# Optimization experiments

Measured on AMD Instinct MI355X. Metric: run time of the kernel, lower is better.

Reference implementation:

```python
import jax, jax.numpy as jnp
import numpy as np

B, S, D = 4, 4096, 1024
H = 16
HD = D // H
L = 4
MLP_MULT = 4
MAX_CHUNKS = 1024
ROPE_BASE = 10000.0


def _rms(x):
    eps = jnp.asarray(jnp.finfo(x.dtype).eps, x.dtype)
    return x * jax.lax.rsqrt(jnp.mean(x * x, axis=-1, keepdims=True) + eps)


def _rope_tables(seq_len, dim):
    inv = 1.0 / ROPE_BASE ** (np.arange(0, dim, 2, dtype=np.float32) / dim)
    t = np.arange(seq_len, dtype=np.float32)
    freqs = np.outer(t, inv)  # [T, dim/2]
    return jnp.asarray(np.cos(freqs)), jnp.asarray(np.sin(freqs))


def _apply_rope(x, cos, sin):
    # x: [B,H,T,hd]; cos/sin: [T, hd/2]
    half = x.shape[-1] // 2
    x1, x2 = x[..., :half], x[..., half:]
    c = cos[None, None, :, :]
    s = sin[None, None, :, :]
    return jnp.concatenate([x1 * c + x2 * s, -x1 * s + x2 * c], axis=-1)


def chunk_reduce(x, boundary_hard, max_chunks):
    # x: [B,S,D]; boundary_hard: [B,S] in {0,1}, boundary_hard[:,0]==1
    ids = jnp.cumsum(boundary_hard.astype(jnp.int32), axis=1) - 1  # [B,S]
    seg = lambda xb, ib: jax.ops.segment_sum(xb, ib, num_segments=max_chunks)
    sums = jax.vmap(seg)(x, ids)                                   # [B,C,D]
    counts = jax.vmap(seg)(jnp.ones(x.shape[:2], x.dtype)[..., None].swapaxes(0, 0), ids) if False else jax.vmap(seg)(jnp.ones((x.shape[0], x.shape[1], 1), x.dtype), ids)
    latents = sums / jnp.maximum(counts, 1.0)
    num_chunks = ids[:, -1] + 1
    valid = jnp.arange(max_chunks)[None, :] < num_chunks[:, None]
    return latents, ids, valid


def _attn(x, wq, wk, wv, wo, qg, cos, sin):
    b, t, _ = x.shape
    q = (x @ wq.T).reshape(b, t, H, HD).transpose(0, 2, 1, 3)
    k = (x @ wk.T).reshape(b, t, H, HD).transpose(0, 2, 1, 3)
    v = (x @ wv.T).reshape(b, t, H, HD).transpose(0, 2, 1, 3)
    q = _apply_rope(_rms(q), cos, sin)
    k = _apply_rope(_rms(k), cos, sin)
    q = q * qg[None, :, None, None]
    scores = jnp.einsum('bhqd,bhkd->bhqk', q, k) / np.sqrt(HD).astype(np.float32)
    causal = jnp.tril(jnp.ones((t, t), bool))
    scores = jnp.where(causal[None, None], scores, jnp.asarray(-jnp.inf, scores.dtype))
    p = jax.nn.softmax(scores, axis=-1)
    y = jnp.einsum('bhqk,bhkd->bhqd', p, v).transpose(0, 2, 1, 3).reshape(b, t, D)
    return y @ wo.T


def _mlp(x, fc, proj):
    h = jax.nn.relu(x @ fc.T)
    return (h * h) @ proj.T


def reference(x, boundary_hard, Wq, Wk, Wv, Wo, q_gain, fc_w, proj_w,
              attn_scale, mlp_scale, resid_mix, max_chunks):
    latents, _, valid = chunk_reduce(x, boundary_hard, max_chunks)
    cos, sin = _rope_tables(max_chunks, HD)
    x0 = latents
    h = latents
    for l in range(L):
        mix = resid_mix[l]
        h = mix[0][None, None, :] * h + mix[1][None, None, :] * x0
        a = _attn(_rms(h), Wq[l], Wk[l], Wv[l], Wo[l], q_gain[l], cos, sin)
        h = h + attn_scale[l][None, None, :] * a
        h = h + mlp_scale[l][None, None, :] * _mlp(_rms(h), fc_w[l], proj_w[l])
    return h * valid[..., None].astype(h.dtype)


def setup_inputs() -> dict:
    key = jax.random.key(0)
    ks = jax.random.split(key, 12)
    rng = np.random.default_rng(0)
    boundary = np.zeros((B, S), np.int32)
    for b in range(B):
        kcnt = int(rng.integers(MAX_CHUNKS // 2, MAX_CHUNKS - 1))
        pos = rng.choice(S, size=kcnt, replace=False)
        boundary[b, pos] = 1
    boundary[:, 0] = 1
    sd = 0.02
    return {
        'x': jax.random.normal(ks[0], (B, S, D), jnp.float32),
        'boundary_hard': jnp.asarray(boundary),
        'Wq': jax.random.normal(ks[1], (L, D, D), jnp.float32) * sd,
        'Wk': jax.random.normal(ks[2], (L, D, D), jnp.float32) * sd,
        'Wv': jax.random.normal(ks[3], (L, D, D), jnp.float32) * sd,
        'Wo': jax.random.normal(ks[4], (L, D, D), jnp.float32) * sd,
        'q_gain': jnp.ones((L, H), jnp.float32),
        'fc_w': jax.random.normal(ks[5], (L, MLP_MULT * D, D), jnp.float32) * sd,
        'proj_w': jax.random.normal(ks[6], (L, D, MLP_MULT * D), jnp.float32) * sd,
        'attn_scale': jnp.ones((L, D), jnp.float32),
        'mlp_scale': jnp.ones((L, D), jnp.float32),
        'resid_mix': jnp.stack([jnp.ones((L, D)), jnp.zeros((L, D))], axis=1).astype(jnp.float32),
        'max_chunks': MAX_CHUNKS,
    }
```

## Files before the change

kernel.cpp:

```cpp
#include <hip/hip_runtime.h>
#include <math.h>

#define BB   4
#define SS   4096
#define DD   1024
#define HH   16
#define HDIM 64
#define CC   1024
#define DFF  4096
#define LL   4

static constexpr float F32_EPS = 1.1920928955078125e-07f;

typedef __attribute__((ext_vector_type(8))) __bf16 bf16x8;
typedef __attribute__((ext_vector_type(4))) float  f32x4;

__device__ __forceinline__ uint f2bf(float f) {
    uint u = __float_as_uint(f);
    return (u + 0x7fffu + ((u >> 16) & 1u)) >> 16;
}
__device__ __forceinline__ float bf2f(uint u) {
    return __uint_as_float(u << 16);
}

__device__ __forceinline__ void gl_lds16(const ushort* g, ushort* l) {
    __builtin_amdgcn_global_load_lds(
        (const __attribute__((address_space(1))) unsigned int*)g,
        (__attribute__((address_space(3))) unsigned int*)l, 16, 0, 0);
}

__global__ __launch_bounds__(256) void castlayer_kernel(const float* __restrict__ Wq,
                                                        const float* __restrict__ Wk,
                                                        const float* __restrict__ Wv,
                                                        const float* __restrict__ Wo,
                                                        const float* __restrict__ fc,
                                                        const float* __restrict__ proj,
                                                        ushort* __restrict__ out) {
    int i = blockIdx.x * blockDim.x + threadIdx.x;
    const int U = DD * DD / 8;
    const float* src;
    if (i < 3 * U) {
        src = (i < U ? Wq : (i < 2 * U ? Wk : Wv)) + (size_t)(i < U ? i : (i < 2*U ? i-U : i-2*U)) * 8;
    } else if (i < 4 * U) {
        src = Wo + (size_t)(i - 3 * U) * 8;
    } else if (i < 8 * U) {
        src = fc + (size_t)(i - 4 * U) * 8;
    } else {
        src = proj + (size_t)(i - 8 * U) * 8;
    }
    const float4* p = (const float4*)src;
    float4 a = p[0], b = p[1];
    uint4 o;
    o.x = f2bf(a.x) | (f2bf(a.y) << 16);
    o.y = f2bf(a.z) | (f2bf(a.w) << 16);
    o.z = f2bf(b.x) | (f2bf(b.y) << 16);
    o.w = f2bf(b.z) | (f2bf(b.w) << 16);
    *(uint4*)(out + (size_t)i * 8) = o;
}

__global__ void rope_init_kernel(float* __restrict__ cosT, float* __restrict__ sinT) {
    int idx = blockIdx.x * blockDim.x + threadIdx.x;
    int pos = idx >> 5;
    int i   = idx & 31;
    float inv = powf(10000.0f, -(float)i / 32.0f);
    float f = (float)pos * inv;
    cosT[idx] = cosf(f);
    sinT[idx] = sinf(f);
}

__global__ __launch_bounds__(1024) void scan_kernel(const int* __restrict__ boundary,
                                                    int* __restrict__ starts,
                                                    int* __restrict__ nch) {
    __shared__ int tmp[1024];
    int b = blockIdx.x, t = threadIdx.x;
    int base = b * SS + t * 4;
    int v0 = boundary[base + 0], v1 = boundary[base + 1];
    int v2 = boundary[base + 2], v3 = boundary[base + 3];
    int p0 = v0, p1 = p0 + v1, p2 = p1 + v2, p3 = p2 + v3;
    tmp[t] = p3;
    __syncthreads();
    for (int off = 1; off < 1024; off <<= 1) {
        int add = (t >= off) ? tmp[t - off] : 0;
        __syncthreads();
        tmp[t] += add;
        __syncthreads();
    }
    int excl = tmp[t] - p3;
    if (v0) starts[b * (CC + 1) + (excl + p0 - 1)] = t * 4 + 0;
    if (v1) starts[b * (CC + 1) + (excl + p1 - 1)] = t * 4 + 1;
    if (v2) starts[b * (CC + 1) + (excl + p2 - 1)] = t * 4 + 2;
    if (v3) starts[b * (CC + 1) + (excl + p3 - 1)] = t * 4 + 3;
    int total = tmp[1023];
    if (t == 0) nch[b] = total;
    for (int c = t; c <= CC; c += 1024)
        if (c >= total) starts[b * (CC + 1) + c] = SS;
}

__global__ __launch_bounds__(256) void latents_kernel(const float* __restrict__ x,
                                                      const int* __restrict__ starts,
                                                      float* __restrict__ h,
                                                      float* __restrict__ x0) {
    int c = blockIdx.x, b = blockIdx.y, t = threadIdx.x;
    int s0 = starts[b * (CC + 1) + c];
    int s1 = starts[b * (CC + 1) + c + 1];
    float a0 = 0.f, a1 = 0.f, a2 = 0.f, a3 = 0.f;
    for (int r = s0; r < s1; ++r) {
        const float4 xv = *(const float4*)&x[((size_t)(b * SS + r)) * DD + t * 4];
        a0 += xv.x; a1 += xv.y; a2 += xv.z; a3 += xv.w;
    }
    float inv = (s1 > s0) ? 1.0f / (float)(s1 - s0) : 0.0f;
    float4 o = make_float4(a0 * inv, a1 * inv, a2 * inv, a3 * inv);
    size_t off = ((size_t)(b * CC + c)) * DD + t * 4;
    *(float4*)&h[off]  = o;
    *(float4*)&x0[off] = o;
}

__global__ __launch_bounds__(256) void rmsmix_kernel(const float* __restrict__ hin,
                                                     const float* __restrict__ x0,
                                                     const float* __restrict__ mix,
                                                     float* __restrict__ hout,
                                                     ushort* __restrict__ xnout) {
    int row = blockIdx.x, t = threadIdx.x;
    size_t off = (size_t)row * DD + t * 4;
    float4 hv = *(const float4*)&hin[off];
    float4 m0 = *(const float4*)&mix[t * 4];
    float4 m1 = *(const float4*)&mix[DD + t * 4];
    float4 xv = *(const float4*)&x0[off];
    hv.x = m0.x * hv.x + m1.x * xv.x;
    hv.y = m0.y * hv.y + m1.y * xv.y;
    hv.z = m0.z * hv.z + m1.z * xv.z;
    hv.w = m0.w * hv.w + m1.w * xv.w;
    float ss = hv.x * hv.x + hv.y * hv.y + hv.z * hv.z + hv.w * hv.w;
    for (int o = 32; o; o >>= 1) ss += __shfl_xor(ss, o);
    __shared__ float wsum[4];
    int lane = t & 63, wid = t >> 6;
    if (lane == 0) wsum[wid] = ss;
    __syncthreads();
    float tot = wsum[0] + wsum[1] + wsum[2] + wsum[3];
    float r = rsqrtf(tot * (1.0f / DD) + F32_EPS);
    *(float4*)&hout[off] = hv;
    uint2 pk;
    pk.x = f2bf(hv.x * r) | (f2bf(hv.y * r) << 16);
    pk.y = f2bf(hv.z * r) | (f2bf(hv.w * r) << 16);
    *(uint2*)&xnout[off] = pk;
}

template <int HASMIX>
__global__ __launch_bounds__(256) void residrms_kernel(float* __restrict__ h,
                                                       const ushort* __restrict__ a0,
                                                       const ushort* __restrict__ a1,
                                                       const float* __restrict__ scale,
                                                       const float* __restrict__ x0,
                                                       const float* __restrict__ mix,
                                                       ushort* __restrict__ xnout) {
    int row = blockIdx.x, t = threadIdx.x;
    size_t off = (size_t)row * DD + t * 4;
    float4 hv = *(const float4*)&h[off];
    uint2 pa = *(const uint2*)&a0[off];
    uint2 pb = *(const uint2*)&a1[off];
    float4 sv = *(const float4*)&scale[t * 4];
    hv.x += sv.x * (bf2f(pa.x & 0xffff) + bf2f(pb.x & 0xffff));
    hv.y += sv.y * (bf2f(pa.x >> 16)    + bf2f(pb.x >> 16));
    hv.z += sv.z * (bf2f(pa.y & 0xffff) + bf2f(pb.y & 0xffff));
    hv.w += sv.w * (bf2f(pa.y >> 16)    + bf2f(pb.y >> 16));
    if (HASMIX) {
        float4 m0 = *(const float4*)&mix[t * 4];
        float4 m1 = *(const float4*)&mix[DD + t * 4];
        float4 xv = *(const float4*)&x0[off];
        hv.x = m0.x * hv.x + m1.x * xv.x;
        hv.y = m0.y * hv.y + m1.y * xv.y;
        hv.z = m0.z * hv.z + m1.z * xv.z;
        hv.w = m0.w * hv.w + m1.w * xv.w;
    }
    float ss = hv.x * hv.x + hv.y * hv.y + hv.z * hv.z + hv.w * hv.w;
    for (int o = 32; o; o >>= 1) ss += __shfl_xor(ss, o);
    __shared__ float wsum[4];
    int lane = t & 63, wid = t >> 6;
    if (lane == 0) wsum[wid] = ss;
    __syncthreads();
    float tot = wsum[0] + wsum[1] + wsum[2] + wsum[3];
    float r = rsqrtf(tot * (1.0f / DD) + F32_EPS);
    *(float4*)&h[off] = hv;
    uint2 pk;
    pk.x = f2bf(hv.x * r) | (f2bf(hv.y * r) << 16);
    pk.y = f2bf(hv.z * r) | (f2bf(hv.w * r) << 16);
    *(uint2*)&xnout[off] = pk;
}

template <int EPI>
__global__ __launch_bounds__(256) void gemm_bf16(const ushort* __restrict__ A,
                                                 const ushort* __restrict__ W,
                                                 ushort* __restrict__ C0,
                                                 ushort* __restrict__ C1,
                                                 ushort* __restrict__ C2,
                                                 int M, int N, int K, int lda, int ldw,
                                                 size_t partStride) {
    __shared__ __align__(16) ushort Als[2][128 * 64];
    __shared__ __align__(16) ushort Wls[2][128 * 64];
    const int tid  = threadIdx.x;
    const int wid  = tid >> 6, lane = tid & 63;
    const int wr   = wid >> 1, wc   = wid & 1;
    const int l15  = lane & 15, lhi = lane >> 4;

    const int gx = gridDim.x, gy = gridDim.y;
    int i = (blockIdx.z * gy + blockIdx.y) * gx + blockIdx.x;
    int G = gx * gy * (int)gridDim.z;
    int v = (i & 7) * (G >> 3) + (i >> 3);
    int mt = v % gy;
    int rest = v / gy;
    int nt = rest % gx;
    int zt = rest / gx;
    const int mbase = mt * 128, nbase = nt * 128;

    A  += (size_t)zt * K;
    W  += (size_t)zt * K;
    C0 += (size_t)zt * partStride;

    const int srow8  = lane >> 3;
    const int gchunk = ((lane & 7) ^ srow8) * 8;
    const ushort* Ag = A + (size_t)(mbase + wid * 32 + srow8) * lda + gchunk;
    const ushort* Wg = W + (size_t)(nbase + wid * 32 + srow8) * ldw + gchunk;
    const int ldsoff = (wid * 32) * 64;

    f32x4 acc[4][4] = {};
    const int swz  = (l15 & 7) << 3;
    const int aoff = (wr * 64 + l15) * 64;
    const int woff = (wc * 64 + l15) * 64;

    auto STAGE = [&](ushort* Alb, ushort* Wlb, int kk) {
#pragma unroll
        for (int s = 0; s < 4; ++s) {
            gl_lds16(Ag + kk + (size_t)s * 8 * lda, Alb + ldsoff + s * 8 * 64);
            gl_lds16(Wg + kk + (size_t)s * 8 * ldw, Wlb + ldsoff + s * 8 * 64);
        }
    };
    auto COMPUTE = [&](const ushort* Ab, const ushort* Wb) {
#pragma unroll
        for (int ks = 0; ks < 2; ++ks) {
            const int fcol = (ks * 32 + lhi * 8) ^ swz;
            bf16x8 af[4], bfm[4];
#pragma unroll
            for (int m = 0; m < 4; ++m)
                af[m] = *(const bf16x8*)(Ab + aoff + m * 1024 + fcol);
#pragma unroll
            for (int n = 0; n < 4; ++n)
                bfm[n] = *(const bf16x8*)(Wb + woff + n * 1024 + fcol);
#pragma unroll
            for (int m = 0; m < 4; ++m)
#pragma unroll
                for (int n = 0; n < 4; ++n)
                    acc[m][n] = __builtin_amdgcn_mfma_f32_16x16x32_bf16(
                        af[m], bfm[n], acc[m][n], 0, 0, 0);
        }
    };

    STAGE(Als[0], Wls[0], 0);
    __syncthreads();
    for (int k0 = 0; k0 < K; k0 += 128) {
        if (k0 + 64 < K) STAGE(Als[1], Wls[1], k0 + 64);
        COMPUTE(Als[0], Wls[0]);
        __syncthreads();
        if (k0 + 128 < K) STAGE(Als[0], Wls[0], k0 + 128);
        COMPUTE(Als[1], Wls[1]);
        __syncthreads();
    }

    ushort* dst = C0;
    int colb = nbase;
    if (EPI == 3) {
        if (nbase < 1024)      { dst = C0; colb = nbase; }
        else if (nbase < 2048) { dst = C1; colb = nbase - 1024; }
        else                   { dst = C2; colb = nbase - 2048; }
    }
    const int ldc = (EPI == 3) ? 1024 : N;
    const int row0 = mbase + wr * 64 + lhi * 4;
    const int col0 = colb + wc * 64 + l15;
#pragma unroll
    for (int m = 0; m < 4; ++m)
#pragma unroll
        for (int n = 0; n < 4; ++n) {
            int cc = col0 + n * 16;
#pragma unroll
            for (int r = 0; r < 4; ++r) {
                int rr = row0 + m * 16 + r;
                float v2 = acc[m][n][r];
                if (EPI == 1) { v2 = fmaxf(v2, 0.0f); v2 = v2 * v2; }
                dst[(size_t)rr * ldc + cc] = (ushort)f2bf(v2);
            }
        }
}

__global__ __launch_bounds__(256) void qknorm2_kernel(ushort* __restrict__ qbuf,
                                                      ushort* __restrict__ kbuf,
                                                      const float* __restrict__ cosT,
                                                      const float* __restrict__ sinT,
                                                      const float* __restrict__ gain) {
    int which = blockIdx.y;
    ushort* dst = which ? kbuf : qbuf;
    int gid = blockIdx.x * blockDim.x + threadIdx.x;
    int gw = gid >> 6, lane = gid & 63;
    int head = gw & (HH - 1);
    int c = (gw >> 4) & (CC - 1);
    int b = gw >> 14;
    size_t off = ((size_t)(b * CC + c)) * DD + head * HDIM + lane;
    float v = bf2f(dst[off]);
    float ss = v * v;
    for (int o = 32; o; o >>= 1) ss += __shfl_xor(ss, o);
    float r = rsqrtf(ss * (1.0f / HDIM) + F32_EPS);
    float vn = v * r;
    float other = __shfl_xor(vn, 32);
    int i = lane & 31;
    float cv = cosT[c * 32 + i], sv = sinT[c * 32 + i];
    float out = (lane < 32) ? (vn * cv + other * sv) : (vn * cv - other * sv);
    if (which == 0) out *= gain[head] * 0.125f;
    dst[off] = (ushort)f2bf(out);
}

__global__ __launch_bounds__(256) void vtrans_kernel(const ushort* __restrict__ v,
                                                     ushort* __restrict__ vt) {
    __shared__ ushort Ls[64][72];
    int kt = blockIdx.x, head = blockIdx.y, b = blockIdx.z;
    int tid = threadIdx.x;
    int r = tid >> 3;
    int ch = (tid & 7) * 8;
#pragma unroll
    for (int s = 0; s < 2; ++s) {
        int kv = r + s * 32;
        int4 t4 = *(const int4*)&v[((size_t)(b * CC + kt * 64 + kv)) * DD + head * HDIM + ch];
        *(int4*)&Ls[kv][ch] = t4;
    }
    __syncthreads();
#pragma unroll
    for (int s = 0; s < 2; ++s) {
        int d = r + s * 32;
        ushort o[8];
#pragma unroll
        for (int j = 0; j < 8; ++j) o[j] = Ls[ch + j][d];
        *(int4*)&vt[((size_t)((b * HH + head) * HDIM + d)) * CC + kt * 64 + ch] = *(int4*)o;
    }
}

__global__ __launch_bounds__(512) void attn_mfma(const ushort* __restrict__ q,
                                                 const ushort* __restrict__ k,
                                                 const ushort* __restrict__ vt,
                                                 ushort* __restrict__ y,
                                                 const float* __restrict__ gain) {
    __shared__ __align__(16) ushort Qs[128 * 64];
    __shared__ __align__(16) ushort Ks[64 * 64];
    __shared__ __align__(16) ushort VT[64 * 64];
    __shared__ __align__(16) ushort Ps[128 * 64];
    const int qt = 7 - blockIdx.x;
    const int head = blockIdx.y, b = blockIdx.z;
    const int tid = threadIdx.x;
    const int wid = tid >> 6, lane = tid & 63;
    const int l15 = lane & 15, lhi = lane >> 4;
    const int wq0 = wid * 16;
    const int qbase = qt * 128;
    const float mstat = 8.0f * fabsf(gain[head]);

    const int srow = tid >> 3;
    const int scol = (tid & 7) * 8;

#pragma unroll
    for (int s = 0; s < 2; ++s) {
        int r = srow + s * 64;
        int4 t4 = *(const int4*)&q[((size_t)(b * CC + qbase + r)) * DD + head * HDIM + scol];
        *(int4*)&Qs[r * 64 + (scol ^ ((r & 7) << 3))] = t4;
    }

    f32x4 oacc[4] = {};
    float lpart[4] = {0.f, 0.f, 0.f, 0.f};

    const int NT = 2 * qt + 2;

    auto LOADK = [&](int4& kr, int4& vr, int kt_) {
        kr = *(const int4*)&k[((size_t)(b * CC + kt_ * 64 + srow)) * DD + head * HDIM + scol];
        vr = *(const int4*)&vt[((size_t)((b * HH + head) * HDIM + srow)) * CC + kt_ * 64 + scol];
    };
    auto WRITEK = [&](const int4& kr, const int4& vr) {
        *(int4*)&Ks[srow * 64 + (scol ^ ((srow & 7) << 3))] = kr;
        *(int4*)&VT[srow * 64 + (scol ^ ((srow & 7) << 3))] = vr;
    };
    auto TILE = [&](int kt) {
        f32x4 sac[4] = {};
        __builtin_amdgcn_s_setprio(1);
#pragma unroll
        for (int ks = 0; ks < 2; ++ks) {
            int dcol = ks * 32 + lhi * 8;
            int arow = wq0 + l15;
            bf16x8 af = *(const bf16x8*)&Qs[arow * 64 + (dcol ^ ((arow & 7) << 3))];
#pragma unroll
            for (int n = 0; n < 4; ++n) {
                int krow = n * 16 + l15;
                bf16x8 bfr = *(const bf16x8*)&Ks[krow * 64 + (dcol ^ ((krow & 7) << 3))];
                sac[n] = __builtin_amdgcn_mfma_f32_16x16x32_bf16(af, bfr, sac[n], 0, 0, 0);
            }
        }
        __builtin_amdgcn_s_setprio(0);

        if (kt >= 2 * qt) {
            const int kb0 = kt * 64;
#pragma unroll
            for (int r = 0; r < 4; ++r) {
                int qrow_g = qbase + wq0 + lhi * 4 + r;
                float p0 = __expf(sac[0][r] - mstat);
                float p1 = __expf(sac[1][r] - mstat);
                float p2 = __expf(sac[2][r] - mstat);
                float p3 = __expf(sac[3][r] - mstat);
                if (kb0 + l15      > qrow_g) p0 = 0.f;
                if (kb0 + 16 + l15 > qrow_g) p1 = 0.f;
                if (kb0 + 32 + l15 > qrow_g) p2 = 0.f;
                if (kb0 + 48 + l15 > qrow_g) p3 = 0.f;
                lpart[r] += (p0 + p1) + (p2 + p3);
                int qrow_l = wq0 + lhi * 4 + r;
                int pb = qrow_l * 64, sw = (qrow_l & 7) << 3;
                Ps[pb + ((l15)      ^ sw)] = (ushort)f2bf(p0);
                Ps[pb + ((16 + l15) ^ sw)] = (ushort)f2bf(p1);
                Ps[pb + ((32 + l15) ^ sw)] = (ushort)f2bf(p2);
                Ps[pb + ((48 + l15) ^ sw)] = (ushort)f2bf(p3);
            }
        } else {
#pragma unroll
            for (int r = 0; r < 4; ++r) {
                float p0 = __expf(sac[0][r] - mstat);
                float p1 = __expf(sac[1][r] - mstat);
                float p2 = __expf(sac[2][r] - mstat);
                float p3 = __expf(sac[3][r] - mstat);
                lpart[r] += (p0 + p1) + (p2 + p3);
                int qrow_l = wq0 + lhi * 4 + r;
                int pb = qrow_l * 64, sw = (qrow_l & 7) << 3;
                Ps[pb + ((l15)      ^ sw)] = (ushort)f2bf(p0);
                Ps[pb + ((16 + l15) ^ sw)] = (ushort)f2bf(p1);
                Ps[pb + ((32 + l15) ^ sw)] = (ushort)f2bf(p2);
                Ps[pb + ((48 + l15) ^ sw)] = (ushort)f2bf(p3);
            }
        }

        __builtin_amdgcn_s_setprio(1);
#pragma unroll
        for (int ks = 0; ks < 2; ++ks) {
            int kcol = ks * 32 + lhi * 8;
            int arow = wq0 + l15;
            bf16x8 pf = *(const bf16x8*)&Ps[arow * 64 + (kcol ^ ((arow & 7) << 3))];
#pragma unroll
            for (int n = 0; n < 4; ++n) {
                int vrow = n * 16 + l15;
                bf16x8 vf = *(const bf16x8*)&VT[vrow * 64 + (kcol ^ ((vrow & 7) << 3))];
                oacc[n] = __builtin_amdgcn_mfma_f32_16x16x32_bf16(pf, vf, oacc[n], 0, 0, 0);
            }
        }
        __builtin_amdgcn_s_setprio(0);
    };

    int4 kra, vra, krb, vrb;
    LOADK(kra, vra, 0);
    for (int kt = 0; kt < NT; kt += 2) {
        __syncthreads();
        WRITEK(kra, vra);
        __syncthreads();
        LOADK(krb, vrb, kt + 1);
        TILE(kt);
        __syncthreads();
        WRITEK(krb, vrb);
        __syncthreads();
        if (kt + 2 < NT) LOADK(kra, vra, kt + 2);
        TILE(kt + 1);
    }

#pragma unroll
    for (int r = 0; r < 4; ++r) {
        float ls = lpart[r];
#pragma unroll
        for (int off = 1; off < 16; off <<= 1) ls += __shfl_xor(ls, off);
        float inv = 1.0f / ls;
        int qrow_g = qbase + wq0 + lhi * 4 + r;
        size_t base = ((size_t)(b * CC + qrow_g)) * DD + head * HDIM;
#pragma unroll
        for (int n = 0; n < 4; ++n)
            y[base + n * 16 + l15] = (ushort)f2bf(oacc[n][r] * inv);
    }
}

__global__ void residmask_kernel(const float* __restrict__ h, const ushort* __restrict__ a0,
                                 const ushort* __restrict__ a1,
                                 const float* __restrict__ scale,
                                 const int* __restrict__ nch,
                                 float* __restrict__ out) {
    int idx = blockIdx.x * blockDim.x + threadIdx.x;
    size_t off = (size_t)idx * 4;
    int c = (idx >> 8) & (CC - 1);
    int b = idx >> 18;
    float4 hv = *(const float4*)&h[off];
    uint2 pa = *(const uint2*)&a0[off];
    uint2 pb = *(const uint2*)&a1[off];
    float4 sv = *(const float4*)&scale[(idx & 255) * 4];
    hv.x += sv.x * (bf2f(pa.x & 0xffff) + bf2f(pb.x & 0xffff));
    hv.y += sv.y * (bf2f(pa.x >> 16)    + bf2f(pb.x >> 16));
    hv.z += sv.z * (bf2f(pa.y & 0xffff) + bf2f(pb.y & 0xffff));
    hv.w += sv.w * (bf2f(pa.y >> 16)    + bf2f(pb.y >> 16));
    if (c >= nch[b]) hv = make_float4(0.f, 0.f, 0.f, 0.f);
    *(float4*)&out[off] = hv;
}

extern "C" void kernel_launch(void* const* d_in, const int* in_sizes, int n_in,
                              void* d_out, int out_size, void* d_ws, size_t ws_size,
                              hipStream_t stream) {
    const float* x        = (const float*)d_in[0];
    const int*   boundary = (const int*)d_in[1];
    const float* Wq       = (const float*)d_in[2];
    const float* Wk       = (const float*)d_in[3];
    const float* Wv       = (const float*)d_in[4];
    const float* Wo       = (const float*)d_in[5];
    const float* qg       = (const float*)d_in[6];
    const float* fcw      = (const float*)d_in[7];
    const float* projw    = (const float*)d_in[8];
    const float* ascale   = (const float*)d_in[9];
    const float* mscale   = (const float*)d_in[10];
    const float* rmix     = (const float*)d_in[11];
    float* out = (float*)d_out;

    const size_t NTOK = (size_t)BB * CC * DD;
    const size_t NHID = (size_t)BB * CC * DFF;
    const size_t D2   = (size_t)DD * DD;

    float* ws   = (float*)d_ws;
    float*  h    = ws;
    float*  x0   = h  + NTOK;
    float*  pbf  = x0 + NTOK;
    float*  spare= pbf + NTOK;
    ushort* xnb  = (ushort*)(spare + NTOK);
    ushort* ybf  = xnb + NTOK;
    ushort* hidb = ybf + NTOK;
    ushort* wbuf = hidb + NHID;
    ushort* vtb  = wbuf + NHID;
    float*  cosT = (float*)(vtb + NTOK);
    float*  sinT = cosT + (size_t)CC * 32;
    int*    starts = (int*)(sinT + (size_t)CC * 32);
    int*    nch    = starts + BB * (CC + 1);

    ushort* pb0 = (ushort*)pbf;
    ushort* pb1 = pb0 + NTOK;

    ushort* qbb = hidb;
    ushort* kbb = hidb + NTOK;
    ushort* vbb = hidb + 2 * NTOK;

    ushort* wqkv = wbuf;
    ushort* wwo  = wbuf + 3 * D2;
    ushort* wfc  = wbuf + 4 * D2;
    ushort* wpj  = wbuf + 8 * D2;

    const int M = BB * CC;
    const int CASTL = (int)(12 * D2 / 8 / 256);

    rope_init_kernel<<<CC * 32 / 256, 256, 0, stream>>>(cosT, sinT);
    scan_kernel<<<BB, 1024, 0, stream>>>(boundary, starts, nch);
    latents_kernel<<<dim3(CC, BB), 256, 0, stream>>>(x, starts, h, x0);
    rmsmix_kernel<<<M, 256, 0, stream>>>(h, x0, rmix, h, xnb);

    for (int l = 0; l < LL; ++l) {
        castlayer_kernel<<<CASTL, 256, 0, stream>>>(Wq + l * D2, Wk + l * D2, Wv + l * D2,
                                                    Wo + l * D2,
                                                    fcw + (size_t)l * DFF * DD,
                                                    projw + (size_t)l * DD * DFF, wbuf);
        gemm_bf16<3><<<dim3(3 * DD / 128, M / 128, 1), 256, 0, stream>>>(
            xnb, wqkv, qbb, kbb, vbb, M, 3 * DD, DD, DD, DD, 0);
        qknorm2_kernel<<<dim3((BB * CC * HH * 64) / 256, 2), 256, 0, stream>>>(
            qbb, kbb, cosT, sinT, qg + l * HH);
        vtrans_kernel<<<dim3(CC / 64, HH, BB), 256, 0, stream>>>(vbb, vtb);
        attn_mfma<<<dim3(8, HH, BB), 512, 0, stream>>>(qbb, kbb, vtb, ybf, qg + l * HH);
        gemm_bf16<0><<<dim3(DD / 128, M / 128, 2), 256, 0, stream>>>(
            ybf, wwo, pb0, nullptr, nullptr, M, DD, DD / 2, DD, DD, NTOK);
        residrms_kernel<0><<<M, 256, 0, stream>>>(h, pb0, pb1, ascale + l * DD,
                                                  nullptr, nullptr, xnb);
        gemm_bf16<1><<<dim3(DFF / 128, M / 128, 1), 256, 0, stream>>>(
            xnb, wfc, hidb, nullptr, nullptr, M, DFF, DD, DD, DD, 0);
        gemm_bf16<0><<<dim3(DD / 128, M / 128, 2), 256, 0, stream>>>(
            hidb, wpj, pb0, nullptr, nullptr, M, DD, DFF / 2, DFF, DFF, NTOK);
        if (l < LL - 1) {
            residrms_kernel<1><<<M, 256, 0, stream>>>(h, pb0, pb1, mscale + l * DD,
                                                      x0, rmix + (size_t)(l + 1) * 2 * DD, xnb);
        } else {
            residmask_kernel<<<(int)(NTOK / 4 / 256), 256, 0, stream>>>(
                h, pb0, pb1, mscale + l * DD, nch, out);
        }
    }
}
```

Baseline: 952.6 us.

## Fuse QK RMSNorm and RoPE into QKV GEMM epilogue, use 512-thread GEMM blocks

The QKV GEMM epilogue now computes per-head RMS normalization, RoPE rotation and the query gain/scale in registers, using cross-lane shuffles over the 16 lanes that hold a 64-wide head. This removes the separate qknorm2 pass that re-read and re-wrote Q and K. All GEMMs also switch from 4 to 8 waves per 128x128 tile, so each wave holds a 32x64 sub-tile and half the accumulators, trading register pressure for more waves per block. The epilogue reads cos/sin tables per row, which adds scattered loads.

```diff
diff --git a/kernel.cpp b/kernel.cpp
--- a/kernel.cpp
+++ b/kernel.cpp
@@ -188,11 +188,14 @@
 }
 
 template <int EPI>
-__global__ __launch_bounds__(256) void gemm_bf16(const ushort* __restrict__ A,
+__global__ __launch_bounds__(512) void gemm_bf16(const ushort* __restrict__ A,
                                                  const ushort* __restrict__ W,
                                                  ushort* __restrict__ C0,
                                                  ushort* __restrict__ C1,
                                                  ushort* __restrict__ C2,
+                                                 const float* __restrict__ cosT,
+                                                 const float* __restrict__ sinT,
+                                                 const float* __restrict__ gain,
                                                  int M, int N, int K, int lda, int ldw,
                                                  size_t partStride) {
     __shared__ __align__(16) ushort Als[2][128 * 64];
@@ -218,18 +221,18 @@
 
     const int srow8  = lane >> 3;
     const int gchunk = ((lane & 7) ^ srow8) * 8;
-    const ushort* Ag = A + (size_t)(mbase + wid * 32 + srow8) * lda + gchunk;
-    const ushort* Wg = W + (size_t)(nbase + wid * 32 + srow8) * ldw + gchunk;
-    const int ldsoff = (wid * 32) * 64;
-
-    f32x4 acc[4][4] = {};
+    const ushort* Ag = A + (size_t)(mbase + wid * 16 + srow8) * lda + gchunk;
+    const ushort* Wg = W + (size_t)(nbase + wid * 16 + srow8) * ldw + gchunk;
+    const int ldsoff = (wid * 16) * 64;
+
+    f32x4 acc[2][4] = {};
     const int swz  = (l15 & 7) << 3;
-    const int aoff = (wr * 64 + l15) * 64;
+    const int aoff = (wr * 32 + l15) * 64;
     const int woff = (wc * 64 + l15) * 64;
 
     auto STAGE = [&](ushort* Alb, ushort* Wlb, int kk) {
 #pragma unroll
-        for (int s = 0; s < 4; ++s) {
+        for (int s = 0; s < 2; ++s) {
             gl_lds16(Ag + kk + (size_t)s * 8 * lda, Alb + ldsoff + s * 8 * 64);
             gl_lds16(Wg + kk + (size_t)s * 8 * ldw, Wlb + ldsoff + s * 8 * 64);
         }
@@ -238,15 +241,15 @@
 #pragma unroll
         for (int ks = 0; ks < 2; ++ks) {
             const int fcol = (ks * 32 + lhi * 8) ^ swz;
-            bf16x8 af[4], bfm[4];
-#pragma unroll
-            for (int m = 0; m < 4; ++m)
+            bf16x8 af[2], bfm[4];
+#pragma unroll
+            for (int m = 0; m < 2; ++m)
                 af[m] = *(const bf16x8*)(Ab + aoff + m * 1024 + fcol);
 #pragma unroll
             for (int n = 0; n < 4; ++n)
                 bfm[n] = *(const bf16x8*)(Wb + woff + n * 1024 + fcol);
 #pragma unroll
-            for (int m = 0; m < 4; ++m)
+            for (int m = 0; m < 2; ++m)
 #pragma unroll
                 for (int n = 0; n < 4; ++n)
                     acc[m][n] = __builtin_amdgcn_mfma_f32_16x16x32_bf16(
@@ -265,55 +268,68 @@
         __syncthreads();
     }
 
-    ushort* dst = C0;
-    int colb = nbase;
+    const int row0 = mbase + wr * 32 + lhi * 4;
+
     if (EPI == 3) {
-        if (nbase < 1024)      { dst = C0; colb = nbase; }
-        else if (nbase < 2048) { dst = C1; colb = nbase - 1024; }
-        else                   { dst = C2; colb = nbase - 2048; }
-    }
-    const int ldc = (EPI == 3) ? 1024 : N;
-    const int row0 = mbase + wr * 64 + lhi * 4;
-    const int col0 = colb + wc * 64 + l15;
-#pragma unroll
-    for (int m = 0; m < 4; ++m)
-#pragma unroll
-        for (int n = 0; n < 4; ++n) {
-            int cc = col0 + n * 16;
-#pragma unroll
-            for (int r = 0; r < 4; ++r) {
-                int rr = row0 + m * 16 + r;
-                float v2 = acc[m][n][r];
-                if (EPI == 1) { v2 = fmaxf(v2, 0.0f); v2 = v2 * v2; }
-                dst[(size_t)rr * ldc + cc] = (ushort)f2bf(v2);
+        const int third = nbase >> 10;
+        const int bandbase = (nbase & 1023) + wc * 64;
+        ushort* dst = (third == 0) ? C0 : (third == 1 ? C1 : C2);
+        if (third == 2) {
+#pragma unroll
+            for (int m = 0; m < 2; ++m)
+#pragma unroll
+                for (int n = 0; n < 4; ++n)
+#pragma unroll
+                    for (int r = 0; r < 4; ++r) {
+                        int rr = row0 + m * 16 + r;
+                        dst[(size_t)rr * 1024 + bandbase + n * 16 + l15] =
+                            (ushort)f2bf(acc[m][n][r]);
+                    }
+        } else {
+            const int hd = bandbase >> 6;
+            const float g = (third == 0) ? gain[hd] * 0.125f : 1.0f;
+#pragma unroll
+            for (int m = 0; m < 2; ++m)
+#pragma unroll
+                for (int r = 0; r < 4; ++r) {
+                    int rr = row0 + m * 16 + r;
+                    float v0 = acc[m][0][r], v1 = acc[m][1][r];
+                    float v2 = acc[m][2][r], v3 = acc[m][3][r];
+                    float ss = v0 * v0 + v1 * v1 + v2 * v2 + v3 * v3;
+#pragma unroll
+                    for (int off = 1; off < 16; off <<= 1) ss += __shfl_xor(ss, off);
+                    float rn = rsqrtf(ss * (1.0f / HDIM) + F32_EPS);
+                    v0 *= rn; v1 *= rn; v2 *= rn; v3 *= rn;
+                    int c = rr & (CC - 1);
+                    float c0 = cosT[c * 32 + l15],      s0 = sinT[c * 32 + l15];
+                    float c1 = cosT[c * 32 + 16 + l15], s1 = sinT[c * 32 + 16 + l15];
+                    float o0 = (v0 * c0 + v2 * s0) * g;
+                    float o1 = (v1 * c1 + v3 * s1) * g;
+                    float o2 = (v2 * c0 - v0 * s0) * g;
+                    float o3 = (v3 * c1 - v1 * s1) * g;
+                    size_t rbase = (size_t)rr * 1024 + bandbase;
+                    dst[rbase + l15]      = (ushort)f2bf(o0);
+                    dst[rbase + 16 + l15] = (ushort)f2bf(o1);
+                    dst[rbase + 32 + l15] = (ushort)f2bf(o2);
+                    dst[rbase + 48 + l15] = (ushort)f2bf(o3);
+                }
+        }
+    } else {
+        const int col0 = nbase + wc * 64 + l15;
+#pragma unroll
+        for (int m = 0; m < 2; ++m)
+#pragma unroll
+            for (int n = 0; n < 4; ++n) {
+                int cc = col0 + n * 16;
+#pragma unroll
+                for (int r = 0; r < 4; ++r) {
+                    int rr = row0 + m * 16 + r;
+                    float v2 = acc[m][n][r];
+                    if (EPI == 1) { v2 = fmaxf(v2, 0.0f); v2 = v2 * v2; }
+                    C0[(size_t)rr * N + cc] = (ushort)f2bf(v2);
+                }
             }
-        }
-}
-
-__global__ __launch_bounds__(256) void qknorm2_kernel(ushort* __restrict__ qbuf,
-                                                      ushort* __restrict__ kbuf,
-                                                      const float* __restrict__ cosT,
-                                                      const float* __restrict__ sinT,
-                                                      const float* __restrict__ gain) {
-    int which = blockIdx.y;
-    ushort* dst = which ? kbuf : qbuf;
-    int gid = blockIdx.x * blockDim.x + threadIdx.x;
-    int gw = gid >> 6, lane = gid & 63;
-    int head = gw & (HH - 1);
-    int c = (gw >> 4) & (CC - 1);
-    int b = gw >> 14;
-    size_t off = ((size_t)(b * CC + c)) * DD + head * HDIM + lane;
-    float v = bf2f(dst[off]);
-    float ss = v * v;
-    for (int o = 32; o; o >>= 1) ss += __shfl_xor(ss, o);
-    float r = rsqrtf(ss * (1.0f / HDIM) + F32_EPS);
-    float vn = v * r;
-    float other = __shfl_xor(vn, 32);
-    int i = lane & 31;
-    float cv = cosT[c * 32 + i], sv = sinT[c * 32 + i];
-    float out = (lane < 32) ? (vn * cv + other * sv) : (vn * cv - other * sv);
-    if (which == 0) out *= gain[head] * 0.125f;
-    dst[off] = (ushort)f2bf(out);
+    }
 }
 
 __global__ __launch_bounds__(256) void vtrans_kernel(const ushort* __restrict__ v,
@@ -563,20 +579,21 @@
                                                     Wo + l * D2,
                                                     fcw + (size_t)l * DFF * DD,
                                                     projw + (size_t)l * DD * DFF, wbuf);
-        gemm_bf16<3><<<dim3(3 * DD / 128, M / 128, 1), 256, 0, stream>>>(
-            xnb, wqkv, qbb, kbb, vbb, M, 3 * DD, DD, DD, DD, 0);
-        qknorm2_kernel<<<dim3((BB * CC * HH * 64) / 256, 2), 256, 0, stream>>>(
-            qbb, kbb, cosT, sinT, qg + l * HH);
+        gemm_bf16<3><<<dim3(3 * DD / 128, M / 128, 1), 512, 0, stream>>>(
+            xnb, wqkv, qbb, kbb, vbb, cosT, sinT, qg + l * HH, M, 3 * DD, DD, DD, DD, 0);
         vtrans_kernel<<<dim3(CC / 64, HH, BB), 256, 0, stream>>>(vbb, vtb);
         attn_mfma<<<dim3(8, HH, BB), 512, 0, stream>>>(qbb, kbb, vtb, ybf, qg + l * HH);
-        gemm_bf16<0><<<dim3(DD / 128, M / 128, 2), 256, 0, stream>>>(
-            ybf, wwo, pb0, nullptr, nullptr, M, DD, DD / 2, DD, DD, NTOK);
+        gemm_bf16<0><<<dim3(DD / 128, M / 128, 2), 512, 0, stream>>>(
+            ybf, wwo, pb0, nullptr, nullptr, nullptr, nullptr, nullptr,
+            M, DD, DD / 2, DD, DD, NTOK);
         residrms_kernel<0><<<M, 256, 0, stream>>>(h, pb0, pb1, ascale + l * DD,
                                                   nullptr, nullptr, xnb);
-        gemm_bf16<1><<<dim3(DFF / 128, M / 128, 1), 256, 0, stream>>>(
-            xnb, wfc, hidb, nullptr, nullptr, M, DFF, DD, DD, DD, 0);
-        gemm_bf16<0><<<dim3(DD / 128, M / 128, 2), 256, 0, stream>>>(
-            hidb, wpj, pb0, nullptr, nullptr, M, DD, DFF / 2, DFF, DFF, NTOK);
+        gemm_bf16<1><<<dim3(DFF / 128, M / 128, 1), 512, 0, stream>>>(
+            xnb, wfc, hidb, nullptr, nullptr, nullptr, nullptr, nullptr,
+            M, DFF, DD, DD, DD, 0);
+        gemm_bf16<0><<<dim3(DD / 128, M / 128, 2), 512, 0, stream>>>(
+            hidb, wpj, pb0, nullptr, nullptr, nullptr, nullptr, nullptr,
+            M, DD, DFF / 2, DFF, DFF, NTOK);
         if (l < LL - 1) {
             residrms_kernel<1><<<M, 256, 0, stream>>>(h, pb0, pb1, mscale + l * DD,
                                                       x0, rmix + (size_t)(l + 1) * 2 * DD, xnb);
```

New measurement: 847.2 us (median of 2 runs). -11.1%, faster.
